# Kernel tuning notes

Measured on AMD Instinct MI355X. Metric: run time of the kernel, lower is better.

The kernel has to match this reference:

```python
import jax, jax.numpy as jnp
import numpy as np
import math

DIM = 4096
DV = 1024          # compress_dim
H = 16             # num_heads
NS = 32            # num_seeds
B, L = 8, 2048
EPS = 1e-5


def _layernorm(x, g, b):
    mu = jnp.mean(x, axis=-1, keepdims=True)
    var = jnp.mean((x - mu) ** 2, axis=-1, keepdims=True)
    return (x - mu) * jax.lax.rsqrt(var + EPS) * g + b


def setup_inputs() -> dict:
    key = jax.random.key(0)
    ks = jax.random.split(key, 12)
    def lin(k, out_d, in_d):
        scale = math.sqrt(6.0 / (in_d + out_d))  # xavier_uniform
        return jax.random.uniform(k, (out_d, in_d), jnp.float32, -scale, scale)
    return {
        "X": jax.random.normal(ks[0], (B, L, DIM), jnp.float32),
        "pad_mask": jax.random.randint(ks[1], (B, L), 0, 2, jnp.int32),
        "S": jax.random.uniform(ks[2], (1, NS, DV), jnp.float32, -0.05, 0.05),
        "Wq": lin(ks[3], DV, DV), "bq": jnp.zeros((DV,), jnp.float32),
        "Wk": lin(ks[4], DV, DIM), "bk": jnp.zeros((DV,), jnp.float32),
        "Wv": lin(ks[5], DV, DIM), "bv": jnp.zeros((DV,), jnp.float32),
        "Wo": lin(ks[6], DV, DV), "bo": jnp.zeros((DV,), jnp.float32),
        "g0": jnp.ones((DV,), jnp.float32), "beta0": jnp.zeros((DV,), jnp.float32),
        "g1": jnp.ones((DV,), jnp.float32), "beta1": jnp.zeros((DV,), jnp.float32),
    }


def reference(X, pad_mask, S, Wq, bq, Wk, bk, Wv, bv, Wo, bo, g0, beta0, g1, beta1):
    b, l, _ = X.shape
    dh = DV // H
    scale = 1.0 / math.sqrt(DV)  # NOTE: full dim_V, not per-head dim
    Q = jnp.broadcast_to(S, (b, NS, DV))              # seeds repeated per batch
    Qp = (Q @ Wq.T + bq).reshape(b, NS, H, dh)
    Kp = (X @ Wk.T + bk).reshape(b, l, H, dh)
    Vp = (X @ Wv.T + bv).reshape(b, l, H, dh)
    score = jnp.einsum('bqhd,bkhd->bhqk', Qp, Kp) * scale
    m = (pad_mask != 0)[:, None, None, :]             # [b,1,1,k]
    score = jnp.where(m, score, jnp.float32(-1e12))
    A = jax.nn.softmax(score, axis=-1) * m.astype(score.dtype)  # post-softmax renorm
    O = jnp.einsum('bhqk,bkhd->bqhd', A, Vp).reshape(b, NS, DV)
    O = Q + O
    O = _layernorm(O, g0, beta0)
    O = O + jax.nn.relu(O @ Wo.T + bo)
    O = _layernorm(O, g1, beta1)
    return O
```

## Files before the change

### kernel.cpp

```cpp
#include <hip/hip_runtime.h>

#define DIMX 4096
#define DVX  1024
#define HX   16
#define DHX  64
#define NSX  32
#define BX   8
#define LX   2048
#define EPSF 1e-5f

typedef unsigned short u16;
typedef unsigned int   u32;

using bf16x8 = __attribute__((ext_vector_type(8))) __bf16;
using f32x4  = __attribute__((ext_vector_type(4))) float;

__device__ __forceinline__ float bfu(u16 u) {
    union { u32 i; float f; } c; c.i = ((u32)u) << 16; return c.f;
}
__device__ __forceinline__ u16 f2b(float f) {
    union { float f; u32 u; } c; c.f = f;
    u32 u = c.u;
    u32 r = (u + 0x7fffu + ((u >> 16) & 1u)) >> 16;
    return (u16)r;
}

__device__ __forceinline__ void async16(const u16* g, u16* l) {
    __builtin_amdgcn_global_load_lds(
        (const __attribute__((address_space(1))) void*)g,
        (__attribute__((address_space(3))) void*)l, 16, 0, 0);
}

template<bool ISF>
__device__ __forceinline__ void ld8(const void* base, size_t idx, float o[8]) {
    if (ISF) {
        const float* f = (const float*)base + idx;
        float4 a = *(const float4*)f, b = *(const float4*)(f + 4);
        o[0]=a.x; o[1]=a.y; o[2]=a.z; o[3]=a.w;
        o[4]=b.x; o[5]=b.y; o[6]=b.z; o[7]=b.w;
    } else {
        const u16* h = (const u16*)base + idx;
        uint4 v = *(const uint4*)h;
        o[0]=bfu(v.x & 0xffff); o[1]=bfu(v.x >> 16);
        o[2]=bfu(v.y & 0xffff); o[3]=bfu(v.y >> 16);
        o[4]=bfu(v.z & 0xffff); o[5]=bfu(v.z >> 16);
        o[6]=bfu(v.w & 0xffff); o[7]=bfu(v.w >> 16);
    }
}
__device__ __forceinline__ float ld1(const void* base, size_t idx, bool isf) {
    return isf ? ((const float*)base)[idx] : bfu(((const u16*)base)[idx]);
}

__global__ __launch_bounds__(256) void detect_kernel(const u16* __restrict__ X,
                                                     int* __restrict__ flag) {
    __shared__ int cnt;
    if (threadIdx.x == 0) cnt = 0;
    __syncthreads();
    int local = 0;
    for (int i = threadIdx.x; i < 8192; i += 256) {
        u32 e = ((u32)X[i] >> 7) & 0xffu;
        if (e >= 200u) local++;
    }
    atomicAdd(&cnt, local);
    __syncthreads();
    if (threadIdx.x == 0) *flag = (cnt > 32) ? 1 : 0;
}

__global__ __launch_bounds__(256) void cvt_kernel(const int* __restrict__ flag,
                                                  const float* __restrict__ src,
                                                  u16* __restrict__ dst, int ngrp) {
    if (*flag == 0) return;
    int stride = gridDim.x * 256;
    for (int i = blockIdx.x * 256 + threadIdx.x; i < ngrp; i += stride) {
        const float4* f = (const float4*)(src + (size_t)i * 8);
        float4 a = f[0], b = f[1];
        uint4 r;
        r.x = (u32)f2b(a.x) | ((u32)f2b(a.y) << 16);
        r.y = (u32)f2b(a.z) | ((u32)f2b(a.w) << 16);
        r.z = (u32)f2b(b.x) | ((u32)f2b(b.y) << 16);
        r.w = (u32)f2b(b.z) | ((u32)f2b(b.w) << 16);
        *(uint4*)(dst + (size_t)i * 8) = r;
    }
}

__global__ __launch_bounds__(256) void qp_kernel(
        const int* __restrict__ flag, const void* __restrict__ S,
        const void* __restrict__ Wq, const void* __restrict__ bq,
        float* __restrict__ Qp) {
    int wid = blockIdx.x * 4 + (threadIdx.x >> 6);
    int lane = threadIdx.x & 63;
    int q = wid >> 10, n = wid & 1023;
    bool isf = (*flag != 0);
    float p = 0.f;
    if (isf) {
        const float4* s4 = (const float4*)((const float*)S + (size_t)q * DVX);
        const float4* w4 = (const float4*)((const float*)Wq + (size_t)n * DVX);
#pragma unroll
        for (int e = 0; e < 4; e++) {
            float4 a = s4[e * 64 + lane];
            float4 b = w4[e * 64 + lane];
            p += a.x * b.x + a.y * b.y + a.z * b.z + a.w * b.w;
        }
    } else {
        const u16* srow = (const u16*)S + (size_t)q * DVX + lane * 16;
        const u16* wrow = (const u16*)Wq + (size_t)n * DVX + lane * 16;
#pragma unroll
        for (int c = 0; c < 2; c++) {
            uint4 a = *(const uint4*)(srow + c * 8);
            uint4 b = *(const uint4*)(wrow + c * 8);
            p += bfu(a.x & 0xffff) * bfu(b.x & 0xffff) + bfu(a.x >> 16) * bfu(b.x >> 16)
               + bfu(a.y & 0xffff) * bfu(b.y & 0xffff) + bfu(a.y >> 16) * bfu(b.y >> 16)
               + bfu(a.z & 0xffff) * bfu(b.z & 0xffff) + bfu(a.z >> 16) * bfu(b.z >> 16)
               + bfu(a.w & 0xffff) * bfu(b.w & 0xffff) + bfu(a.w >> 16) * bfu(b.w >> 16);
        }
    }
#pragma unroll
    for (int off = 32; off > 0; off >>= 1)
        p += __shfl_xor(p, off, 64);
    if (lane == 0) Qp[wid] = p + ld1(bq, n, isf);
}

__global__ __launch_bounds__(512, 2) void kv_gemm3(
        const int* __restrict__ flag, int boffs,
        const void* __restrict__ X,  const u16* __restrict__ Xb,
        const void* __restrict__ Wk, const void* __restrict__ bk,
        const void* __restrict__ Wv, const void* __restrict__ bv,
        const u16* __restrict__ Wkb, const u16* __restrict__ Wvb,
        u16* __restrict__ Kp, u16* __restrict__ Vp) {
    extern __shared__ __align__(16) u16 lds[];
    const bool isf = (*flag != 0);
    const u16* Xs = isf ? Xb : (const u16*)X;

    const int t = threadIdx.x;
    const int lane = t & 63, w = t >> 6;
    const int wm = w >> 2, wn = w & 3;
    const int quad = lane >> 4, l16 = lane & 15;
    const int l8 = l16 & 7;

    const int bid = blockIdx.x + boffs;
    const int swz = (bid & 7) * 64 + (bid >> 3);
    const int mt = swz >> 3, nt = swz & 7;
    const int m0 = mt * 256, n0 = nt * 256;

    const u16* Wb16; const void* bias; int boff;
    if (n0 < DVX) { Wb16 = (isf ? Wkb : (const u16*)Wk) + (size_t)n0 * DIMX;
                    bias = bk; boff = n0; }
    else          { Wb16 = (isf ? Wvb : (const u16*)Wv) + (size_t)(n0 - DVX) * DIMX;
                    bias = bv; boff = n0 - DVX; }

    f32x4 acc[8][4];
#pragma unroll
    for (int i = 0; i < 8; i++)
#pragma unroll
        for (int j = 0; j < 4; j++) acc[i][j] = {0.f, 0.f, 0.f, 0.f};

    {
        u16* An = lds;
        u16* Bn = lds + 32768;
#pragma unroll
        for (int i = 0; i < 4; i++) {
            int gi = i * 512 + t;
            int r = gi >> 3;
            int g = (gi & 7) ^ (r & 7);
            async16(Xs + (size_t)(m0 + r) * DIMX + g * 8, An + gi * 8);
        }
#pragma unroll
        for (int i = 0; i < 4; i++) {
            int gi = i * 512 + t;
            int r = gi >> 3;
            int g = (gi & 7) ^ (r & 7);
            async16(Wb16 + (size_t)r * DIMX + g * 8, Bn + gi * 8);
        }
        asm volatile("s_waitcnt vmcnt(0)" ::: "memory");
        __builtin_amdgcn_s_barrier();
    }

    for (int kt = 0; kt < DIMX / 64; kt++) {
        u16* Ab = lds + (kt & 1) * 16384;
        u16* Bb = lds + 32768 + (kt & 1) * 16384;
        u16* An = lds + ((kt + 1) & 1) * 16384;
        u16* Bn = lds + 32768 + ((kt + 1) & 1) * 16384;
        const int k1 = (kt + 1) * 64;

        if (kt + 1 < DIMX / 64) {
#pragma unroll
            for (int i = 0; i < 4; i++) {
                int gi = i * 512 + t;
                int r = gi >> 3;
                int g = (gi & 7) ^ (r & 7);
                async16(Xs + (size_t)(m0 + r) * DIMX + k1 + g * 8, An + gi * 8);
            }
#pragma unroll
            for (int i = 0; i < 4; i++) {
                int gi = i * 512 + t;
                int r = gi >> 3;
                int g = (gi & 7) ^ (r & 7);
                async16(Wb16 + (size_t)r * DIMX + k1 + g * 8, Bn + gi * 8);
            }
        }
        __builtin_amdgcn_sched_barrier(0);

        bf16x8 bfr[4][2];
#pragma unroll
        for (int ni = 0; ni < 4; ni++)
#pragma unroll
            for (int ks = 0; ks < 2; ks++) {
                int R = wn * 64 + ni * 16 + l16;
                int cc = ((ks * 4 + quad) ^ l8);
                bfr[ni][ks] = *(const bf16x8*)&Bb[R * 64 + cc * 8];
            }

#pragma unroll
        for (int p = 0; p < 4; p++) {
            bf16x8 a[2][2];
#pragma unroll
            for (int dm = 0; dm < 2; dm++)
#pragma unroll
                for (int ks = 0; ks < 2; ks++) {
                    int R = wm * 128 + (2 * p + dm) * 16 + l16;
                    int cc = ((ks * 4 + quad) ^ l8);
                    a[dm][ks] = *(const bf16x8*)&Ab[R * 64 + cc * 8];
                }
            __builtin_amdgcn_s_setprio(1);
#pragma unroll
            for (int dm = 0; dm < 2; dm++)
#pragma unroll
                for (int ni = 0; ni < 4; ni++)
#pragma unroll
                    for (int ks = 0; ks < 2; ks++)
                        acc[2 * p + dm][ni] = __builtin_amdgcn_mfma_f32_16x16x32_bf16(
                            a[dm][ks], bfr[ni][ks], acc[2 * p + dm][ni], 0, 0, 0);
            __builtin_amdgcn_s_setprio(0);
        }

        __builtin_amdgcn_sched_barrier(0);
        asm volatile("s_waitcnt vmcnt(0)" ::: "memory");
        __builtin_amdgcn_s_barrier();
        __builtin_amdgcn_sched_barrier(0);
    }

    float bb[4];
#pragma unroll
    for (int ni = 0; ni < 4; ni++)
        bb[ni] = ld1(bias, (size_t)(boff + wn * 64 + ni * 16 + l16), isf);
#pragma unroll
    for (int mi = 0; mi < 8; mi++) {
#pragma unroll
        for (int ni = 0; ni < 4; ni++) {
            int colT = wn * 64 + ni * 16 + l16;
#pragma unroll
            for (int r = 0; r < 4; r++) {
                int rowT = wm * 128 + mi * 16 + quad * 4 + r;
                lds[rowT * 256 + colT] = f2b(acc[mi][ni][r] + bb[ni]);
            }
        }
    }
    __syncthreads();
    {
        u16* dst; int dcol0;
        if (n0 < DVX) { dst = Kp; dcol0 = n0; }
        else          { dst = Vp; dcol0 = n0 - DVX; }
#pragma unroll
        for (int it = 0; it < 16; it++) {
            int idx = it * 512 + t;
            int rowT = idx >> 5;
            int chk = idx & 31;
            uint4 v = *(const uint4*)&lds[rowT * 256 + chk * 8];
            *(uint4*)&dst[(size_t)(m0 + rowT) * DVX + dcol0 + chk * 8] = v;
        }
    }
}

#define TM 128
#define TN 128
#define BKK 32
#define LDT 32

__device__ __forceinline__ uint4 pack8(float o[8]) {
    uint4 r;
    r.x = (u32)f2b(o[0]) | ((u32)f2b(o[1]) << 16);
    r.y = (u32)f2b(o[2]) | ((u32)f2b(o[3]) << 16);
    r.z = (u32)f2b(o[4]) | ((u32)f2b(o[5]) << 16);
    r.w = (u32)f2b(o[6]) | ((u32)f2b(o[7]) << 16);
    return r;
}

__global__ __launch_bounds__(256) void kv_gemm2(
        const int* __restrict__ flag,
        const void* __restrict__ X,  const u16* __restrict__ Xb,
        const void* __restrict__ Wk, const void* __restrict__ bk,
        const void* __restrict__ Wv, const void* __restrict__ bv,
        const u16* __restrict__ Wkb, const u16* __restrict__ Wvb,
        u16* __restrict__ Kp, u16* __restrict__ Vp) {
    __shared__ u16 As[TM * LDT];
    __shared__ u16 Bs[TN * LDT];
    const bool isf = (*flag != 0);
    const u16* Xs = isf ? Xb : (const u16*)X;

    const int t = threadIdx.x;
    const int lane = t & 63, w = t >> 6;
    const int wm = w >> 1, wn = w & 1;
    const int quad = lane >> 4, l16 = lane & 15;
    const int bl = blockIdx.x;
    const int xcd = bl & 7, bq = bl >> 3;
    const int m0 = (xcd + 8 * (bq >> 4)) * TM;
    const int n0 = (bq & 15) * TN;
    const u16* Wb16; const void* bias; int boff;
    if (n0 < DVX) { Wb16 = (isf ? Wkb : (const u16*)Wk) + (size_t)n0 * DIMX;
                    bias = bk; boff = n0; }
    else          { Wb16 = (isf ? Wvb : (const u16*)Wv) + (size_t)(n0 - DVX) * DIMX;
                    bias = bv; boff = n0 - DVX; }

    f32x4 acc[4][4];
#pragma unroll
    for (int i = 0; i < 4; i++)
#pragma unroll
        for (int j = 0; j < 4; j++) acc[i][j] = {0.f, 0.f, 0.f, 0.f};

    const int srow = lane >> 2;
    const int gcol = ((lane & 3) ^ ((lane >> 3) & 3)) * 8;
    const int ph = (l16 >> 1) & 3;

    for (int k0 = 0; k0 < DIMX; k0 += BKK) {
        __syncthreads();
#pragma unroll
        for (int c = 0; c < 2; c++) {
            int rr = w * 32 + c * 16;
            async16(Xs + (size_t)(m0 + rr + srow) * DIMX + k0 + gcol,
                    As + rr * LDT);
            async16(Wb16 + (size_t)(rr + srow) * DIMX + k0 + gcol,
                    Bs + rr * LDT);
        }
        __syncthreads();
        bf16x8 af[4], bfr[4];
#pragma unroll
        for (int mi = 0; mi < 4; mi++) {
            int ar = wm * 64 + mi * 16 + l16;
            af[mi] = *(const bf16x8*)&As[ar * LDT + (quad ^ ph) * 8];
        }
#pragma unroll
        for (int ni = 0; ni < 4; ni++) {
            int br = wn * 64 + ni * 16 + l16;
            bfr[ni] = *(const bf16x8*)&Bs[br * LDT + (quad ^ ph) * 8];
        }
#pragma unroll
        for (int mi = 0; mi < 4; mi++)
#pragma unroll
            for (int ni = 0; ni < 4; ni++)
                acc[mi][ni] = __builtin_amdgcn_mfma_f32_16x16x32_bf16(
                    af[mi], bfr[ni], acc[mi][ni], 0, 0, 0);
    }

#pragma unroll
    for (int mi = 0; mi < 4; mi++) {
#pragma unroll
        for (int ni = 0; ni < 4; ni++) {
            int colL = wn * 64 + ni * 16 + l16;
            int col = n0 + colL;
            float bb = ld1(bias, (size_t)(boff + colL), isf);
            u16* dst; int dcol;
            if (col < DVX) { dst = Kp; dcol = col; }
            else           { dst = Vp; dcol = col - DVX; }
#pragma unroll
            for (int r = 0; r < 4; r++) {
                int row = m0 + wm * 64 + mi * 16 + quad * 4 + r;
                dst[(size_t)row * DVX + dcol] = f2b(acc[mi][ni][r] + bb);
            }
        }
    }
}

template<bool ISF>
__device__ void kv_body(const void* __restrict__ X,
                        const void* __restrict__ Wk, const void* __restrict__ bk,
                        const void* __restrict__ Wv, const void* __restrict__ bv,
                        u16* __restrict__ Kp, u16* __restrict__ Vp,
                        u16* As, u16* Bs) {
    const int t = threadIdx.x;
    const int lane = t & 63, w = t >> 6;
    const int wm = w >> 1, wn = w & 1;
    const int quad = lane >> 4, l16 = lane & 15;
    const int bl = blockIdx.x;
    const int xcd = bl & 7, bq = bl >> 3;
    const int m0 = (xcd + 8 * (bq >> 4)) * TM;
    const int n0 = (bq & 15) * TN;
    const void* Wbase; const void* bias; int boff;
    size_t woff;
    if (n0 < DVX) { Wbase = Wk; bias = bk; woff = (size_t)n0 * DIMX; boff = n0; }
    else          { Wbase = Wv; bias = bv; woff = (size_t)(n0 - DVX) * DIMX; boff = n0 - DVX; }
    const u16* Wb16 = (const u16*)Wbase + woff;
    const float* Wbf = (const float*)Wbase + woff;

    f32x4 acc[4][4];
#pragma unroll
    for (int i = 0; i < 4; i++)
#pragma unroll
        for (int j = 0; j < 4; j++) acc[i][j] = {0.f, 0.f, 0.f, 0.f};

    const int srow = lane >> 2;
    const int gcol = ((lane & 3) ^ ((lane >> 3) & 3)) * 8;
    const int ph = (l16 >> 1) & 3;
    const int r0 = t >> 2, c0 = (t & 3) * 8;
    const int r1 = r0 + 64;
    const int swc = (((t & 3) ^ ((r0 >> 1) & 3))) * 8;

    for (int k0 = 0; k0 < DIMX; k0 += BKK) {
        if constexpr (ISF) {
            float oa0[8], oa1[8], ob0[8], ob1[8];
            ld8<true>(X,   (size_t)(m0 + r0) * DIMX + k0 + c0, oa0);
            ld8<true>(X,   (size_t)(m0 + r1) * DIMX + k0 + c0, oa1);
            ld8<true>(Wbf, (size_t)r0 * DIMX + k0 + c0, ob0);
            ld8<true>(Wbf, (size_t)r1 * DIMX + k0 + c0, ob1);
            __syncthreads();
            *(uint4*)&As[r0 * LDT + swc] = pack8(oa0);
            *(uint4*)&As[r1 * LDT + swc] = pack8(oa1);
            *(uint4*)&Bs[r0 * LDT + swc] = pack8(ob0);
            *(uint4*)&Bs[r1 * LDT + swc] = pack8(ob1);
        } else {
            __syncthreads();
#pragma unroll
            for (int c = 0; c < 2; c++) {
                int rr = w * 32 + c * 16;
                async16((const u16*)X + (size_t)(m0 + rr + srow) * DIMX + k0 + gcol,
                        As + rr * LDT);
                async16(Wb16 + (size_t)(rr + srow) * DIMX + k0 + gcol,
                        Bs + rr * LDT);
            }
        }
        __syncthreads();
        bf16x8 af[4], bfr[4];
#pragma unroll
        for (int mi = 0; mi < 4; mi++) {
            int ar = wm * 64 + mi * 16 + l16;
            af[mi] = *(const bf16x8*)&As[ar * LDT + (quad ^ ph) * 8];
        }
#pragma unroll
        for (int ni = 0; ni < 4; ni++) {
            int br = wn * 64 + ni * 16 + l16;
            bfr[ni] = *(const bf16x8*)&Bs[br * LDT + (quad ^ ph) * 8];
        }
#pragma unroll
        for (int mi = 0; mi < 4; mi++)
#pragma unroll
            for (int ni = 0; ni < 4; ni++)
                acc[mi][ni] = __builtin_amdgcn_mfma_f32_16x16x32_bf16(
                    af[mi], bfr[ni], acc[mi][ni], 0, 0, 0);
    }

#pragma unroll
    for (int mi = 0; mi < 4; mi++) {
#pragma unroll
        for (int ni = 0; ni < 4; ni++) {
            int colL = wn * 64 + ni * 16 + l16;
            int col = n0 + colL;
            float bb = ld1(bias, (size_t)(boff + colL), ISF);
            u16* dst; int dcol;
            if (col < DVX) { dst = Kp; dcol = col; }
            else           { dst = Vp; dcol = col - DVX; }
#pragma unroll
            for (int r = 0; r < 4; r++) {
                int row = m0 + wm * 64 + mi * 16 + quad * 4 + r;
                dst[(size_t)row * DVX + dcol] = f2b(acc[mi][ni][r] + bb);
            }
        }
    }
}

__global__ __launch_bounds__(256) void kv_gemm(
        const int* __restrict__ flag, const void* __restrict__ X,
        const void* __restrict__ Wk, const void* __restrict__ bk,
        const void* __restrict__ Wv, const void* __restrict__ bv,
        u16* __restrict__ Kp, u16* __restrict__ Vp) {
    __shared__ u16 As[TM * LDT];
    __shared__ u16 Bs[TN * LDT];
    if (*flag) kv_body<true>(X, Wk, bk, Wv, bv, Kp, Vp, As, Bs);
    else       kv_body<false>(X, Wk, bk, Wv, bv, Kp, Vp, As, Bs);
}

#define CHK 256
#define NCH (LX / CHK)
__global__ __launch_bounds__(256) void attn2_kernel(
        const float* __restrict__ Qp, const u16* __restrict__ Kp,
        const u16* __restrict__ Vp, const int* __restrict__ pad,
        float* __restrict__ Opart, float* __restrict__ Ml) {
    __shared__ float sc[NSX * CHK];
    const int blk = blockIdx.x;
    const int b  = blk / (HX * NCH);
    const int h  = (blk / NCH) % HX;
    const int c0 = blk % NCH;
    const int t = threadIdx.x;
    const int w = t >> 6, lane = t & 63;
    const int rsub = lane >> 3;
    const int dsub = lane & 7;
    const int q0w = w * 8;

    float qc[8][8];
#pragma unroll
    for (int qq = 0; qq < 8; qq++) {
        const float* qp = Qp + (size_t)(q0w + qq) * DVX + h * DHX + dsub * 8;
        float4 a = *(const float4*)qp, bq4 = *(const float4*)(qp + 4);
        qc[qq][0]=a.x; qc[qq][1]=a.y; qc[qq][2]=a.z; qc[qq][3]=a.w;
        qc[qq][4]=bq4.x; qc[qq][5]=bq4.y; qc[qq][6]=bq4.z; qc[qq][7]=bq4.w;
    }

    const u16* kb = Kp + ((size_t)b * LX + c0 * CHK) * DVX + h * DHX;
    const int* pb = pad + b * LX + c0 * CHK;

    float lmax[8];
#pragma unroll
    for (int qq = 0; qq < 8; qq++) lmax[qq] = -3e38f;
    for (int i = 0; i < CHK / 8; i++) {
        int k = i * 8 + rsub;
        uint4 v = *(const uint4*)(kb + (size_t)k * DVX + dsub * 8);
        float kf[8];
        kf[0]=bfu(v.x & 0xffff); kf[1]=bfu(v.x >> 16);
        kf[2]=bfu(v.y & 0xffff); kf[3]=bfu(v.y >> 16);
        kf[4]=bfu(v.z & 0xffff); kf[5]=bfu(v.z >> 16);
        kf[6]=bfu(v.w & 0xffff); kf[7]=bfu(v.w >> 16);
        int pm = pb[k];
#pragma unroll
        for (int qq = 0; qq < 8; qq++) {
            float s = kf[0]*qc[qq][0] + kf[1]*qc[qq][1]
                    + kf[2]*qc[qq][2] + kf[3]*qc[qq][3]
                    + kf[4]*qc[qq][4] + kf[5]*qc[qq][5]
                    + kf[6]*qc[qq][6] + kf[7]*qc[qq][7];
            s += __shfl_xor(s, 1, 64);
            s += __shfl_xor(s, 2, 64);
            s += __shfl_xor(s, 4, 64);
            s *= 0.03125f;
            s = pm ? s : -1e30f;
            if (dsub == 0) sc[(q0w + qq) * CHK + k] = s;
            lmax[qq] = fmaxf(lmax[qq], s);
        }
    }
#pragma unroll
    for (int qq = 0; qq < 8; qq++) {
        lmax[qq] = fmaxf(lmax[qq], __shfl_xor(lmax[qq], 8, 64));
        lmax[qq] = fmaxf(lmax[qq], __shfl_xor(lmax[qq], 16, 64));
        lmax[qq] = fmaxf(lmax[qq], __shfl_xor(lmax[qq], 32, 64));
    }

#pragma unroll
    for (int qq = 0; qq < 8; qq++) {
        float m = lmax[qq];
        float lsum = 0.f;
#pragma unroll
        for (int it = 0; it < CHK / 64; it++) {
            int idx = (q0w + qq) * CHK + it * 64 + lane;
            float sv = sc[idx];
            float e = (sv > -1e29f) ? __expf(sv - m) : 0.f;
            sc[idx] = e;
            lsum += e;
        }
#pragma unroll
        for (int off = 32; off > 0; off >>= 1)
            lsum += __shfl_xor(lsum, off, 64);
        if (lane == 0) {
            Ml[(size_t)blk * 64 + (q0w + qq) * 2 + 0] = m;
            Ml[(size_t)blk * 64 + (q0w + qq) * 2 + 1] = lsum;
        }
    }

    float acc[8][8];
#pragma unroll
    for (int qq = 0; qq < 8; qq++)
#pragma unroll
        for (int e = 0; e < 8; e++) acc[qq][e] = 0.f;
    const u16* vb = Vp + ((size_t)b * LX + c0 * CHK) * DVX + h * DHX + dsub * 8;
    for (int i = 0; i < CHK / 8; i++) {
        int k = i * 8 + rsub;
        uint4 v = *(const uint4*)(vb + (size_t)k * DVX);
        float vf[8];
        vf[0]=bfu(v.x & 0xffff); vf[1]=bfu(v.x >> 16);
        vf[2]=bfu(v.y & 0xffff); vf[3]=bfu(v.y >> 16);
        vf[4]=bfu(v.z & 0xffff); vf[5]=bfu(v.z >> 16);
        vf[6]=bfu(v.w & 0xffff); vf[7]=bfu(v.w >> 16);
#pragma unroll
        for (int qq = 0; qq < 8; qq++) {
            float p = sc[(q0w + qq) * CHK + k];
#pragma unroll
            for (int e = 0; e < 8; e++) acc[qq][e] += p * vf[e];
        }
    }
#pragma unroll
    for (int qq = 0; qq < 8; qq++) {
#pragma unroll
        for (int e = 0; e < 8; e++) {
            acc[qq][e] += __shfl_xor(acc[qq][e], 8, 64);
            acc[qq][e] += __shfl_xor(acc[qq][e], 16, 64);
            acc[qq][e] += __shfl_xor(acc[qq][e], 32, 64);
        }
        if (rsub == qq) {
            float* op = Opart + ((size_t)blk * NSX + q0w + qq) * DHX + dsub * 8;
            float4 r0 = {acc[qq][0], acc[qq][1], acc[qq][2], acc[qq][3]};
            float4 r1 = {acc[qq][4], acc[qq][5], acc[qq][6], acc[qq][7]};
            *(float4*)op = r0;
            *(float4*)(op + 4) = r1;
        }
    }
}

__global__ __launch_bounds__(256) void attn_combine(
        const float* __restrict__ Opart, const float* __restrict__ Ml,
        float* __restrict__ Oat) {
    const int bh = blockIdx.x;
    const int b = bh / HX, h = bh % HX;
    const int t = threadIdx.x;
    const int q = t >> 3, d0 = (t & 7) * 8;
    const size_t cbase = (size_t)bh * NCH;
    float m = -3e38f;
#pragma unroll
    for (int c = 0; c < NCH; c++)
        m = fmaxf(m, Ml[(cbase + c) * 64 + q * 2]);
    float l = 0.f, o[8];
#pragma unroll
    for (int e = 0; e < 8; e++) o[e] = 0.f;
#pragma unroll
    for (int c = 0; c < NCH; c++) {
        float mc = Ml[(cbase + c) * 64 + q * 2 + 0];
        float lc = Ml[(cbase + c) * 64 + q * 2 + 1];
        float wgt = (mc > -1e29f) ? __expf(mc - m) : 0.f;
        l += wgt * lc;
        const float* op = Opart + ((cbase + c) * NSX + q) * DHX + d0;
        float4 x = *(const float4*)op, y = *(const float4*)(op + 4);
        o[0] += wgt * x.x; o[1] += wgt * x.y; o[2] += wgt * x.z; o[3] += wgt * x.w;
        o[4] += wgt * y.x; o[5] += wgt * y.y; o[6] += wgt * y.z; o[7] += wgt * y.w;
    }
    float inv = (l > 0.f) ? 1.f / l : 0.f;
    float* dst = Oat + ((size_t)(b * NSX) + q) * DVX + h * DHX + d0;
    float4 r0 = {o[0]*inv, o[1]*inv, o[2]*inv, o[3]*inv};
    float4 r1 = {o[4]*inv, o[5]*inv, o[6]*inv, o[7]*inv};
    *(float4*)dst = r0;
    *(float4*)(dst + 4) = r1;
}

#define QG 4
__global__ __launch_bounds__(256) void attn_kernel(
        const float* __restrict__ Qp, const u16* __restrict__ Kp,
        const u16* __restrict__ Vp, const int* __restrict__ pad,
        float* __restrict__ Oat) {
    __shared__ float qv[QG * DHX];
    __shared__ float sc[QG * LX];
    __shared__ float rpart[256 * 8];
    __shared__ float invs[QG];
    const int blk = blockIdx.x;
    const int nqg = NSX / QG;
    const int b  = blk / (HX * nqg);
    const int h  = (blk / nqg) % HX;
    const int q0 = (blk % nqg) * QG;
    const int t = threadIdx.x;
    const int w = t >> 6, lane = t & 63;

    qv[t] = Qp[(size_t)(q0 + (t >> 6)) * DVX + h * DHX + (t & 63)];
    __syncthreads();

    const u16* Kb = Kp + (size_t)b * LX * DVX + h * DHX;
    const int rsub = lane >> 3;
    const int dsub = lane & 7;
    float qc[8];
#pragma unroll
    for (int e = 0; e < 8; e++) qc[e] = qv[w * DHX + dsub * 8 + e];

    float lmax = -3e38f;
    for (int i = 0; i < LX / 8; i++) {
        int k = i * 8 + rsub;
        uint4 v = *(const uint4*)(Kb + (size_t)k * DVX + dsub * 8);
        float s = bfu(v.x & 0xffff) * qc[0] + bfu(v.x >> 16) * qc[1]
                + bfu(v.y & 0xffff) * qc[2] + bfu(v.y >> 16) * qc[3]
                + bfu(v.z & 0xffff) * qc[4] + bfu(v.z >> 16) * qc[5]
                + bfu(v.w & 0xffff) * qc[6] + bfu(v.w >> 16) * qc[7];
        s += __shfl_xor(s, 1, 64);
        s += __shfl_xor(s, 2, 64);
        s += __shfl_xor(s, 4, 64);
        s *= 0.03125f;
        s = (pad[b * LX + k] != 0) ? s : -1e30f;
        if (dsub == 0) sc[w * LX + k] = s;
        lmax = fmaxf(lmax, s);
    }
#pragma unroll
    for (int off = 32; off > 0; off >>= 1)
        lmax = fmaxf(lmax, __shfl_xor(lmax, off, 64));
    float lsum = 0.f;
    for (int i = 0; i < LX / 64; i++) {
        int k = i * 64 + lane;
        float sv = sc[w * LX + k];
        float e = (sv > -1e29f) ? __expf(sv - lmax) : 0.f;
        sc[w * LX + k] = e;
        lsum += e;
    }
#pragma unroll
    for (int off = 32; off > 0; off >>= 1)
        lsum += __shfl_xor(lsum, off, 64);
    if (lane == 0) invs[w] = (lsum > 0.f) ? 1.f / lsum : 0.f;

    const int kg = (t >> 3) & 7, dg = t & 7;
    const u16* Vb = Vp + (size_t)b * LX * DVX + h * DHX + dg * 8;
    float a8[8];
#pragma unroll
    for (int e = 0; e < 8; e++) a8[e] = 0.f;
    for (int i = 0; i < LX / 8; i++) {
        int k = i * 8 + kg;
        float p = sc[w * LX + k];
        uint4 v = *(const uint4*)(Vb + (size_t)k * DVX);
        a8[0] += p * bfu(v.x & 0xffff); a8[1] += p * bfu(v.x >> 16);
        a8[2] += p * bfu(v.y & 0xffff); a8[3] += p * bfu(v.y >> 16);
        a8[4] += p * bfu(v.z & 0xffff); a8[5] += p * bfu(v.z >> 16);
        a8[6] += p * bfu(v.w & 0xffff); a8[7] += p * bfu(v.w >> 16);
    }
#pragma unroll
    for (int e = 0; e < 8; e++) rpart[t * 8 + e] = a8[e];
    __syncthreads();

    {
        int q = t >> 6, d = t & 63;
        float o = 0.f;
#pragma unroll
        for (int g = 0; g < 8; g++)
            o += rpart[(q * 64 + g * 8 + (d >> 3)) * 8 + (d & 7)];
        o *= invs[q];
        Oat[((size_t)(b * NSX + q0 + q)) * DVX + h * DHX + d] = o;
    }
}

template<bool ISF>
__device__ void epi_body(float* u, float* y0, float* red,
                         const float* __restrict__ Oat, const void* __restrict__ S,
                         const void* __restrict__ Wo, const void* __restrict__ bo,
                         const void* __restrict__ g0, const void* __restrict__ be0,
                         const void* __restrict__ g1, const void* __restrict__ be1,
                         void* __restrict__ out) {
    const int bq = blockIdx.x;
    const int q = bq & 31;
    const int t = threadIdx.x;
    const int w = t >> 6, lane = t & 63;

    float ls = 0.f, ls2 = 0.f;
#pragma unroll
    for (int j = 0; j < 2; j++) {
        int c = t + 512 * j;
        float v = ld1(S, (size_t)q * DVX + c, ISF) + Oat[(size_t)bq * DVX + c];
        u[c] = v; ls += v; ls2 += v * v;
    }
    red[t] = ls; __syncthreads();
    for (int s2 = 256; s2 > 0; s2 >>= 1) { if (t < s2) red[t] += red[t + s2]; __syncthreads(); }
    float mu = red[0] / DVX; __syncthreads();
    red[t] = ls2; __syncthreads();
    for (int s2 = 256; s2 > 0; s2 >>= 1) { if (t < s2) red[t] += red[t + s2]; __syncthreads(); }
    float var = red[0] / DVX - mu * mu;
    float r = rsqrtf(var + EPSF);
    __syncthreads();
#pragma unroll
    for (int j = 0; j < 2; j++) {
        int c = t + 512 * j;
        y0[c] = (u[c] - mu) * r * ld1(g0, c, ISF) + ld1(be0, c, ISF);
    }
    __syncthreads();

    float yr[16];
    if constexpr (ISF) {
        const float4* y4 = (const float4*)y0;
#pragma unroll
        for (int e = 0; e < 4; e++) {
            float4 v = y4[e * 64 + lane];
            yr[e*4+0]=v.x; yr[e*4+1]=v.y; yr[e*4+2]=v.z; yr[e*4+3]=v.w;
        }
    } else {
#pragma unroll
        for (int e = 0; e < 8; e++) { yr[e] = y0[lane * 8 + e]; yr[8 + e] = y0[512 + lane * 8 + e]; }
    }
    for (int i = 0; i < 128; i++) {
        int n = i * 8 + w;
        float p = 0.f;
        if constexpr (ISF) {
            const float4* row4 = (const float4*)((const float*)Wo + (size_t)n * DVX);
#pragma unroll
            for (int e = 0; e < 4; e++) {
                float4 wv = row4[e * 64 + lane];
                p += wv.x * yr[e*4] + wv.y * yr[e*4+1]
                   + wv.z * yr[e*4+2] + wv.w * yr[e*4+3];
            }
        } else {
            const uint4* row = (const uint4*)((const u16*)Wo + (size_t)n * DVX);
            uint4 v0 = row[lane], v1 = row[lane + 64];
            p += bfu(v0.x & 0xffff) * yr[0] + bfu(v0.x >> 16) * yr[1]
               + bfu(v0.y & 0xffff) * yr[2] + bfu(v0.y >> 16) * yr[3]
               + bfu(v0.z & 0xffff) * yr[4] + bfu(v0.z >> 16) * yr[5]
               + bfu(v0.w & 0xffff) * yr[6] + bfu(v0.w >> 16) * yr[7];
            p += bfu(v1.x & 0xffff) * yr[8]  + bfu(v1.x >> 16) * yr[9]
               + bfu(v1.y & 0xffff) * yr[10] + bfu(v1.y >> 16) * yr[11]
               + bfu(v1.z & 0xffff) * yr[12] + bfu(v1.z >> 16) * yr[13]
               + bfu(v1.w & 0xffff) * yr[14] + bfu(v1.w >> 16) * yr[15];
        }
#pragma unroll
        for (int off = 32; off > 0; off >>= 1)
            p += __shfl_xor(p, off, 64);
        if (lane == 0) {
            float z = p + ld1(bo, n, ISF);
            u[n] = y0[n] + fmaxf(z, 0.f);
        }
    }
    __syncthreads();
    ls = 0.f; ls2 = 0.f;
#pragma unroll
    for (int j = 0; j < 2; j++) {
        int c = t + 512 * j; float v = u[c]; ls += v; ls2 += v * v;
    }
    red[t] = ls; __syncthreads();
    for (int s2 = 256; s2 > 0; s2 >>= 1) { if (t < s2) red[t] += red[t + s2]; __syncthreads(); }
    mu = red[0] / DVX; __syncthreads();
    red[t] = ls2; __syncthreads();
    for (int s2 = 256; s2 > 0; s2 >>= 1) { if (t < s2) red[t] += red[t + s2]; __syncthreads(); }
    var = red[0] / DVX - mu * mu;
    r = rsqrtf(var + EPSF);
#pragma unroll
    for (int j = 0; j < 2; j++) {
        int c = t + 512 * j;
        float v = (u[c] - mu) * r * ld1(g1, c, ISF) + ld1(be1, c, ISF);
        if (ISF) ((float*)out)[(size_t)bq * DVX + c] = v;
        else     ((u16*)out)[(size_t)bq * DVX + c] = f2b(v);
    }
}

__global__ __launch_bounds__(512) void epi_kernel(
        const int* __restrict__ flag,
        const float* __restrict__ Oat, const void* __restrict__ S,
        const void* __restrict__ Wo, const void* __restrict__ bo,
        const void* __restrict__ g0, const void* __restrict__ be0,
        const void* __restrict__ g1, const void* __restrict__ be1,
        void* __restrict__ out) {
    __shared__ float u[DVX];
    __shared__ float y0[DVX];
    __shared__ float red[512];
    if (*flag) epi_body<true>(u, y0, red, Oat, S, Wo, bo, g0, be0, g1, be1, out);
    else       epi_body<false>(u, y0, red, Oat, S, Wo, bo, g0, be0, g1, be1, out);
}

extern "C" void kernel_launch(void* const* d_in, const int* in_sizes, int n_in,
                              void* d_out, int out_size, void* d_ws, size_t ws_size,
                              hipStream_t stream) {
    (void)in_sizes; (void)n_in; (void)out_size;
    const void* X    = d_in[0];
    const int* pad   = (const int*)d_in[1];
    const void* S    = d_in[2];
    const void* Wq   = d_in[3];
    const void* bq   = d_in[4];
    const void* Wk   = d_in[5];
    const void* bk   = d_in[6];
    const void* Wv   = d_in[7];
    const void* bv   = d_in[8];
    const void* Wo   = d_in[9];
    const void* bo   = d_in[10];
    const void* g0   = d_in[11];
    const void* be0  = d_in[12];
    const void* g1   = d_in[13];
    const void* be1  = d_in[14];

    char* ws = (char*)d_ws;
    int*   flag = (int*)ws;
    float* Qp  = (float*)(ws + 256);
    float* Oat = (float*)(ws + 256 + 131072);
    u16*   Kp  = (u16*)(ws + 256 + 131072 + 1048576);
    u16*   Vp  = Kp + (size_t)BX * LX * DVX;
    u16*   Xb  = Vp + (size_t)BX * LX * DVX;
    u16*   Wkb = Xb + (size_t)BX * LX * DIMX;
    u16*   Wvb = Wkb + (size_t)DVX * DIMX;
    float* Opart = (float*)(Wvb + (size_t)DVX * DIMX);
    float* Ml  = Opart + (size_t)BX * HX * NCH * NSX * DHX;

    size_t need = 256 + 131072 + 1048576
                + 2 * (size_t)BX * LX * DVX * 2
                + (size_t)BX * LX * DIMX * 2
                + 2 * (size_t)DVX * DIMX * 2;
    size_t need2 = need
                 + (size_t)BX * HX * NCH * NSX * DHX * 4
                 + (size_t)BX * HX * NCH * 64 * 4;

    static int attr_ok = -1;
    if (attr_ok < 0) {
        hipError_t e = hipFuncSetAttribute(
            reinterpret_cast<const void*>(kv_gemm3),
            hipFuncAttributeMaxDynamicSharedMemorySize, 131072);
        attr_ok = (e == hipSuccess) ? 1 : 0;
    }

    detect_kernel<<<1, 256, 0, stream>>>((const u16*)X, flag);
    qp_kernel<<<8192, 256, 0, stream>>>(flag, S, Wq, bq, Qp);

    if (ws_size >= need) {
        cvt_kernel<<<2048, 256, 0, stream>>>(flag, (const float*)X, Xb,
                                             BX * LX * DIMX / 8);
        cvt_kernel<<<512, 256, 0, stream>>>(flag, (const float*)Wk, Wkb,
                                            DVX * DIMX / 8);
        cvt_kernel<<<512, 256, 0, stream>>>(flag, (const float*)Wv, Wvb,
                                            DVX * DIMX / 8);
        if (attr_ok == 1) {
            kv_gemm3<<<256, 512, 131072, stream>>>(flag, 0, X, Xb, Wk, bk, Wv, bv,
                                                   Wkb, Wvb, Kp, Vp);
            kv_gemm3<<<256, 512, 131072, stream>>>(flag, 256, X, Xb, Wk, bk, Wv, bv,
                                                   Wkb, Wvb, Kp, Vp);
        } else {
            kv_gemm2<<<2048, 256, 0, stream>>>(flag, X, Xb, Wk, bk, Wv, bv,
                                               Wkb, Wvb, Kp, Vp);
        }
    } else {
        kv_gemm<<<2048, 256, 0, stream>>>(flag, X, Wk, bk, Wv, bv, Kp, Vp);
    }

    if (ws_size >= need2) {
        attn2_kernel<<<BX * HX * NCH, 256, 0, stream>>>(Qp, Kp, Vp, pad,
                                                        Opart, Ml);
        attn_combine<<<BX * HX, 256, 0, stream>>>(Opart, Ml, Oat);
    } else {
        attn_kernel<<<BX * HX * (NSX / QG), 256, 0, stream>>>(Qp, Kp, Vp, pad, Oat);
    }
    epi_kernel<<<BX * NSX, 512, 0, stream>>>(flag, Oat, S, Wo, bo, g0, be0, g1, be1, (void*)d_out);
}
```

Measured before the change: 853.5 us.

## Split epilogue into LN, batched Wo GEMV over 8 rows, and LN kernels

Replaces the single per-row epilogue kernel with three kernels: a first layernorm, a Wo projection that processes 8 rows per block so each Wo row load is reused across 8 outputs, and a final layernorm. The old epilogue reread the full Wo matrix once per output row (256 times). The new path adds two launches and a round trip of intermediates through workspace, and runs only 32 blocks for the GEMV, which may leave most CUs idle.

```diff
diff --git a/kernel.cpp b/kernel.cpp
--- a/kernel.cpp
+++ b/kernel.cpp
@@ -49,6 +49,15 @@
 }
 __device__ __forceinline__ float ld1(const void* base, size_t idx, bool isf) {
     return isf ? ((const float*)base)[idx] : bfu(((const u16*)base)[idx]);
+}
+
+__device__ __forceinline__ float bred256(float x, float* red, int t) {
+#pragma unroll
+    for (int off = 32; off > 0; off >>= 1) x += __shfl_xor(x, off, 64);
+    __syncthreads();
+    if ((t & 63) == 0) red[t >> 6] = x;
+    __syncthreads();
+    return red[0] + red[1] + red[2] + red[3];
 }
 
 __global__ __launch_bounds__(256) void detect_kernel(const u16* __restrict__ X,
@@ -722,6 +731,140 @@
     }
 }
 
+
+__global__ __launch_bounds__(256) void epi_a_kernel(
+        const int* __restrict__ flag, const float* __restrict__ Oat,
+        const void* __restrict__ S, const void* __restrict__ g0,
+        const void* __restrict__ be0, float* __restrict__ y0b) {
+    __shared__ float red[4];
+    const int bq = blockIdx.x, q = bq & 31, t = threadIdx.x;
+    const bool isf = (*flag != 0);
+    float v[4]; float ls = 0.f, ls2 = 0.f;
+#pragma unroll
+    for (int j = 0; j < 4; j++) {
+        int c = t + 256 * j;
+        v[j] = ld1(S, (size_t)q * DVX + c, isf) + Oat[(size_t)bq * DVX + c];
+        ls += v[j]; ls2 += v[j] * v[j];
+    }
+    float mu = bred256(ls, red, t) / DVX;
+    float var = bred256(ls2, red, t) / DVX - mu * mu;
+    float r = rsqrtf(var + EPSF);
+#pragma unroll
+    for (int j = 0; j < 4; j++) {
+        int c = t + 256 * j;
+        y0b[(size_t)bq * DVX + c] = (v[j] - mu) * r * ld1(g0, c, isf) + ld1(be0, c, isf);
+    }
+}
+
+#define EROWS 8
+__global__ __launch_bounds__(512) void epi_b_kernel(
+        const int* __restrict__ flag, const float* __restrict__ y0b,
+        const void* __restrict__ Wo, const void* __restrict__ bo,
+        float* __restrict__ y1b) {
+    const int t = threadIdx.x, w = t >> 6, lane = t & 63;
+    const bool isf = (*flag != 0);
+    const int r0 = blockIdx.x * EROWS;
+
+    float yr[EROWS][16];
+    if (isf) {
+#pragma unroll
+        for (int r = 0; r < EROWS; r++) {
+            const float4* y4 = (const float4*)(y0b + (size_t)(r0 + r) * DVX);
+#pragma unroll
+            for (int e = 0; e < 4; e++) {
+                float4 vv = y4[e * 64 + lane];
+                yr[r][e*4+0]=vv.x; yr[r][e*4+1]=vv.y; yr[r][e*4+2]=vv.z; yr[r][e*4+3]=vv.w;
+            }
+        }
+    } else {
+#pragma unroll
+        for (int r = 0; r < EROWS; r++) {
+            const float* yp = y0b + (size_t)(r0 + r) * DVX;
+#pragma unroll
+            for (int e = 0; e < 8; e++) {
+                yr[r][e] = yp[lane * 8 + e];
+                yr[r][8 + e] = yp[512 + lane * 8 + e];
+            }
+        }
+    }
+
+    for (int i = 0; i < 128; i++) {
+        int n = i * 8 + w;
+        float p[EROWS];
+#pragma unroll
+        for (int r = 0; r < EROWS; r++) p[r] = 0.f;
+        if (isf) {
+            const float4* row4 = (const float4*)((const float*)Wo + (size_t)n * DVX);
+#pragma unroll
+            for (int e = 0; e < 4; e++) {
+                float4 wv = row4[e * 64 + lane];
+#pragma unroll
+                for (int r = 0; r < EROWS; r++)
+                    p[r] += wv.x * yr[r][e*4+0] + wv.y * yr[r][e*4+1]
+                          + wv.z * yr[r][e*4+2] + wv.w * yr[r][e*4+3];
+            }
+        } else {
+            const uint4* row = (const uint4*)((const u16*)Wo + (size_t)n * DVX);
+            uint4 v0 = row[lane], v1 = row[lane + 64];
+            float wf[16];
+            wf[0]=bfu(v0.x & 0xffff);  wf[1]=bfu(v0.x >> 16);
+            wf[2]=bfu(v0.y & 0xffff);  wf[3]=bfu(v0.y >> 16);
+            wf[4]=bfu(v0.z & 0xffff);  wf[5]=bfu(v0.z >> 16);
+            wf[6]=bfu(v0.w & 0xffff);  wf[7]=bfu(v0.w >> 16);
+            wf[8]=bfu(v1.x & 0xffff);  wf[9]=bfu(v1.x >> 16);
+            wf[10]=bfu(v1.y & 0xffff); wf[11]=bfu(v1.y >> 16);
+            wf[12]=bfu(v1.z & 0xffff); wf[13]=bfu(v1.z >> 16);
+            wf[14]=bfu(v1.w & 0xffff); wf[15]=bfu(v1.w >> 16);
+#pragma unroll
+            for (int r = 0; r < EROWS; r++) {
+                float s = 0.f;
+#pragma unroll
+                for (int e = 0; e < 16; e++) s += wf[e] * yr[r][e];
+                p[r] += s;
+            }
+        }
+#pragma unroll
+        for (int r = 0; r < EROWS; r++)
+#pragma unroll
+            for (int off = 32; off > 0; off >>= 1)
+                p[r] += __shfl_xor(p[r], off, 64);
+        if (lane == 0) {
+            float bov = ld1(bo, n, isf);
+#pragma unroll
+            for (int r = 0; r < EROWS; r++) {
+                size_t idx = (size_t)(r0 + r) * DVX + n;
+                y1b[idx] = y0b[idx] + fmaxf(p[r] + bov, 0.f);
+            }
+        }
+    }
+}
+
+__global__ __launch_bounds__(256) void epi_c_kernel(
+        const int* __restrict__ flag, const float* __restrict__ y1b,
+        const void* __restrict__ g1, const void* __restrict__ be1,
+        void* __restrict__ out) {
+    __shared__ float red[4];
+    const int bq = blockIdx.x, t = threadIdx.x;
+    const bool isf = (*flag != 0);
+    float v[4]; float ls = 0.f, ls2 = 0.f;
+#pragma unroll
+    for (int j = 0; j < 4; j++) {
+        int c = t + 256 * j;
+        v[j] = y1b[(size_t)bq * DVX + c];
+        ls += v[j]; ls2 += v[j] * v[j];
+    }
+    float mu = bred256(ls, red, t) / DVX;
+    float var = bred256(ls2, red, t) / DVX - mu * mu;
+    float r = rsqrtf(var + EPSF);
+#pragma unroll
+    for (int j = 0; j < 4; j++) {
+        int c = t + 256 * j;
+        float o = (v[j] - mu) * r * ld1(g1, c, isf) + ld1(be1, c, isf);
+        if (isf) ((float*)out)[(size_t)bq * DVX + c] = o;
+        else     ((u16*)out)[(size_t)bq * DVX + c] = f2b(o);
+    }
+}
+
 template<bool ISF>
 __device__ void epi_body(float* u, float* y0, float* red,
                          const float* __restrict__ Oat, const void* __restrict__ S,
@@ -866,6 +1009,8 @@
     u16*   Wvb = Wkb + (size_t)DVX * DIMX;
     float* Opart = (float*)(Wvb + (size_t)DVX * DIMX);
     float* Ml  = Opart + (size_t)BX * HX * NCH * NSX * DHX;
+    float* y0b = Ml + (size_t)BX * HX * NCH * 64;
+    float* y1b = y0b + (size_t)BX * NSX * DVX;
 
     size_t need = 256 + 131072 + 1048576
                 + 2 * (size_t)BX * LX * DVX * 2
@@ -874,6 +1019,7 @@
     size_t need2 = need
                  + (size_t)BX * HX * NCH * NSX * DHX * 4
                  + (size_t)BX * HX * NCH * 64 * 4;
+    size_t need3 = need2 + 2 * (size_t)BX * NSX * DVX * 4;
 
     static int attr_ok = -1;
     if (attr_ok < 0) {
@@ -913,5 +1059,12 @@
     } else {
         attn_kernel<<<BX * HX * (NSX / QG), 256, 0, stream>>>(Qp, Kp, Vp, pad, Oat);
     }
-    epi_kernel<<<BX * NSX, 512, 0, stream>>>(flag, Oat, S, Wo, bo, g0, be0, g1, be1, (void*)d_out);
-}
+
+    if (ws_size >= need3) {
+        epi_a_kernel<<<BX * NSX, 256, 0, stream>>>(flag, Oat, S, g0, be0, y0b);
+        epi_b_kernel<<<BX * NSX / EROWS, 512, 0, stream>>>(flag, y0b, Wo, bo, y1b);
+        epi_c_kernel<<<BX * NSX, 256, 0, stream>>>(flag, y1b, g1, be1, (void*)d_out);
+    } else {
+        epi_kernel<<<BX * NSX, 512, 0, stream>>>(flag, Oat, S, Wo, bo, g0, be0, g1, be1, (void*)d_out);
+    }
+}
```

Measured after the change: 1.064 ms. 24.7% more time.
